# Kernel optimization log

Measured on AMD Instinct MI355X. Metric: run time of the kernel, lower is better.

Reference implementation:

```python
import jax, jax.numpy as jnp
import numpy as np

H, D = 12, 128          # heads, head_dim
DIM = 1536              # vid_dim == txt_dim == H*D
EPS = 1e-6


def _rmsnorm(x, w):
    # RMSNorm over last dim (head_dim) with learnable scale
    var = jnp.mean(jnp.square(x), axis=-1, keepdims=True)
    return x * jax.lax.rsqrt(var + EPS) * w


def setup_inputs() -> dict:
    key = jax.random.key(0)
    ks = jax.random.split(key, 16)
    B, Lv, Lt = 2, 2 * 24 * 40, 128
    inner = H * D
    s = 0.02
    inp = {
        "vid": jax.random.normal(ks[0], (B * Lv, DIM), jnp.float32),
        "txt": jax.random.normal(ks[1], (B * Lt, DIM), jnp.float32),
        "Wqkv_vid": jax.random.normal(ks[2], (DIM, 3 * inner), jnp.float32) * s,
        "bqkv_vid": jnp.zeros((3 * inner,), jnp.float32),
        "Wqkv_txt": jax.random.normal(ks[3], (DIM, 3 * inner), jnp.float32) * s,
        "bqkv_txt": jnp.zeros((3 * inner,), jnp.float32),
        "nq_vid": jnp.ones((D,), jnp.float32),
        "nk_vid": jnp.ones((D,), jnp.float32),
        "nq_txt": jnp.ones((D,), jnp.float32),
        "nk_txt": jnp.ones((D,), jnp.float32),
        "Wout_vid": jax.random.normal(ks[4], (inner, DIM), jnp.float32) * s,
        "bout_vid": jnp.zeros((DIM,), jnp.float32),
        "Wout_txt": jax.random.normal(ks[5], (inner, DIM), jnp.float32) * s,
        "bout_txt": jnp.zeros((DIM,), jnp.float32),
        # static per-sample shapes (numpy => usable as Python ints under jit)
        "vid_shape": np.array([[2, 24, 40], [2, 24, 40]], np.int64),
        "txt_shape": np.array([[128], [128]], np.int64),
    }
    return inp


def reference(vid, txt, Wqkv_vid, bqkv_vid, Wqkv_txt, bqkv_txt,
              nq_vid, nk_vid, nq_txt, nk_txt,
              Wout_vid, bout_vid, Wout_txt, bout_txt,
              vid_shape, txt_shape):
    B = vid_shape.shape[0]
    Lv = int(np.prod(vid_shape[0]))   # equal lengths across batch
    Lt = int(txt_shape[0, 0])

    # fused QKV projections (separate weights for vid/txt, shared_weights=False)
    vid_qkv = (vid @ Wqkv_vid + bqkv_vid).reshape(-1, 3, H, D)
    txt_qkv = (txt @ Wqkv_txt + bqkv_txt).reshape(-1, 3, H, D)
    vq, vk, vv = vid_qkv[:, 0], vid_qkv[:, 1], vid_qkv[:, 2]
    tq, tk, tv = txt_qkv[:, 0], txt_qkv[:, 1], txt_qkv[:, 2]

    # QK-norm (per-modality RMSNorm over head_dim)
    vq, tq = _rmsnorm(vq, nq_vid), _rmsnorm(tq, nq_txt)
    vk, tk = _rmsnorm(vk, nk_vid), _rmsnorm(tk, nk_txt)

    # multimodal packing: per sample, vid tokens then txt tokens (cu_seqlens over vid_len+txt_len)
    def pack(v, t):
        v = v.reshape(B, Lv, H, D)
        t = t.reshape(B, Lt, H, D)
        return jnp.concatenate([v, t], axis=1)  # [B, Lv+Lt, H, D]

    q = pack(vq, tq).astype(jnp.bfloat16)
    k = pack(vk, tk).astype(jnp.bfloat16)
    v = pack(vv, tv).astype(jnp.bfloat16)

    scale = 1.0 / np.sqrt(D)
    scores = jnp.einsum('blhd,bmhd->bhlm', q, k,
                        preferred_element_type=jnp.float32) * scale
    probs = jax.nn.softmax(scores, axis=-1)
    out = jnp.einsum('bhlm,bmhd->blhd', probs.astype(jnp.bfloat16), v,
                     preferred_element_type=jnp.float32).astype(vid.dtype)

    # unconcat + head merge
    out = out.reshape(B, Lv + Lt, H * D)
    vid_out = out[:, :Lv].reshape(B * Lv, H * D)
    txt_out = out[:, Lv:].reshape(B * Lt, H * D)

    vid_out = vid_out @ Wout_vid + bout_vid
    txt_out = txt_out @ Wout_txt + bout_txt
    return (vid_out, txt_out)
```

## Files before the change

### kernel.cpp

```cpp
#include <hip/hip_runtime.h>
#include <hip/hip_bf16.h>
#include <stdint.h>

typedef __attribute__((ext_vector_type(8))) short  short8;
typedef __attribute__((ext_vector_type(4))) float  f32x4;
typedef __attribute__((ext_vector_type(4))) unsigned int uint4v;
typedef __attribute__((ext_vector_type(4))) unsigned short ushort4v;

#define MFMA16(a,b,c) __builtin_amdgcn_mfma_f32_16x16x32_bf16((a),(b),(c),0,0,0)

#define AS1 __attribute__((address_space(1)))
#define AS3 __attribute__((address_space(3)))
static __device__ __forceinline__ void gload16(void* lds, const void* g) {
  __builtin_amdgcn_global_load_lds((AS1 const void*)g, (AS3 void*)lds, 16, 0, 0);
}

static __device__ __forceinline__ unsigned short f2bf(float x) {
  unsigned int u = __float_as_uint(x);
  u += 0x7fffu + ((u >> 16) & 1u);
  return (unsigned short)(u >> 16);
}
static __device__ __forceinline__ float bf2f(unsigned short h) {
  return __uint_as_float(((unsigned int)h) << 16);
}

#define HDS   12
#define DD    128
#define DIMK  1536
#define NIN   4608
#define LV    1920
#define LT    128
#define LL    2048
#define BB    2
#define MV    3840
#define MT    256
#define MTOT  4096

__global__ __launch_bounds__(256) void split_x(const float* __restrict__ vid,
                                               const float* __restrict__ txt,
                                               unsigned short* __restrict__ xhi) {
  size_t i = ((size_t)blockIdx.x * 256 + threadIdx.x) * 4;
  const size_t NV = (size_t)MV * DIMK;
  const float* src = (i < NV) ? (vid + i) : (txt + (i - NV));
  f32x4 v = *(const f32x4*)src;
  ushort4v hv;
#pragma unroll
  for (int j = 0; j < 4; ++j) hv[j] = f2bf(v[j]);
  *(ushort4v*)(xhi + i) = hv;
}

__global__ __launch_bounds__(256) void transpose_cast(const float* __restrict__ W,
                                                      unsigned short* __restrict__ Thi,
                                                      int K, int N) {
  __shared__ float tile[32][33];
  const int tx = threadIdx.x & 31, ty = threadIdx.x >> 5;
  const int k0 = blockIdx.y * 32, n0 = blockIdx.x * 32;
#pragma unroll
  for (int i = 0; i < 32; i += 8)
    tile[ty + i][tx] = W[(size_t)(k0 + ty + i) * N + n0 + tx];
  __syncthreads();
#pragma unroll
  for (int i = 0; i < 32; i += 8)
    Thi[(size_t)(n0 + ty + i) * K + k0 + tx] = f2bf(tile[tx][ty + i]);
}

__global__ __launch_bounds__(256) void vt_transpose(const unsigned short* __restrict__ v,
                                                    unsigned short* __restrict__ vtb) {
  __shared__ unsigned short tile[32][33];
  const int tx = threadIdx.x & 31, ty = threadIdx.x >> 5;
  const int bh = blockIdx.z;
  const int l0 = blockIdx.x * 32, d0 = blockIdx.y * 32;
  const size_t base = (size_t)bh * LL * DD;
#pragma unroll
  for (int i = 0; i < 32; i += 8)
    tile[ty + i][tx] = v[base + (size_t)(l0 + ty + i) * DD + d0 + tx];
  __syncthreads();
#pragma unroll
  for (int i = 0; i < 32; i += 8)
    vtb[base + (size_t)(d0 + ty + i) * LL + l0 + tx] = tile[tx][ty + i];
}

__device__ __forceinline__ void bf16_mainloop128(
    const unsigned short* __restrict__ Ahi, const unsigned short* __restrict__ Bhi,
    int m0, int n0,
    uint4v* __restrict__ sA, uint4v* __restrict__ sB,
    f32x4 (&acc)[4][4]) {
  const int t = threadIdx.x;
  const int lane = t & 63;
  const int w = t >> 6;
  const int wm = w >> 1, wn = w & 1;
  const int lr = lane & 15, lg = lane >> 4;
  const int sr = t >> 1;
  const int sc = (t & 1) * 2;
  const size_t arow = (size_t)(m0 + sr) * DIMK + sc * 8;
  const size_t brow = (size_t)(n0 + sr) * DIMK + sc * 8;
  const int slot0 = sc * 128 + sr, slot1 = (sc + 1) * 128 + sr;
  const int fA = lg * 128 + wm * 64 + lr;
  const int fB = lg * 128 + wn * 64 + lr;

  uint4v va0 = *(const uint4v*)(Ahi + arow);
  uint4v va1 = *(const uint4v*)(Ahi + arow + 8);
  uint4v vb0 = *(const uint4v*)(Bhi + brow);
  uint4v vb1 = *(const uint4v*)(Bhi + brow + 8);

  int cur = 0;
  for (int k0 = 0; k0 < DIMK; k0 += 32) {
    const int hs = cur * 512;
    sA[hs + slot0] = va0; sA[hs + slot1] = va1;
    sB[hs + slot0] = vb0; sB[hs + slot1] = vb1;
    if (k0 + 32 < DIMK) {
      va0 = *(const uint4v*)(Ahi + arow + k0 + 32);
      va1 = *(const uint4v*)(Ahi + arow + k0 + 40);
      vb0 = *(const uint4v*)(Bhi + brow + k0 + 32);
      vb1 = *(const uint4v*)(Bhi + brow + k0 + 40);
    }
    __syncthreads();
    short8 ah[4], bh[4];
#pragma unroll
    for (int i = 0; i < 4; ++i) {
      ah[i] = *(const short8*)&sA[hs + fA + i * 16];
      bh[i] = *(const short8*)&sB[hs + fB + i * 16];
    }
#pragma unroll
    for (int mi = 0; mi < 4; ++mi)
#pragma unroll
      for (int ni = 0; ni < 4; ++ni)
        acc[mi][ni] = MFMA16(ah[mi], bh[ni], acc[mi][ni]);
    cur ^= 1;
  }
}

__global__ __launch_bounds__(256) void gemm_qkv(
    const unsigned short* __restrict__ Xhi,
    const unsigned short* __restrict__ WvH, const unsigned short* __restrict__ WtH,
    const float* __restrict__ bias_v, const float* __restrict__ bias_t,
    const float* __restrict__ nq_v, const float* __restrict__ nk_v,
    const float* __restrict__ nq_t, const float* __restrict__ nk_t,
    unsigned short* __restrict__ qb, unsigned short* __restrict__ kb,
    unsigned short* __restrict__ vb) {
  __shared__ uint4v sA[1024], sB[1024];
  __shared__ float rowsq[2][128];
  const int t = threadIdx.x;
  const int lane = t & 63;
  const int w = t >> 6;
  const int wm = w >> 1, wn = w & 1;
  const int lr = lane & 15, lg = lane >> 4;
  const int bid = blockIdx.x;
  const int xcd = bid & 7, ii = bid >> 3;
  const int mt = xcd * 4 + (ii & 3), nt = ii >> 2;
  const int m0 = mt * 128, n0 = nt * 128;
  const bool istxt = (m0 >= MV);
  const unsigned short* WThi = istxt ? WtH : WvH;
  const float* bias = istxt ? bias_t : bias_v;
  const int Lmod = istxt ? LT : LV;
  const int loff = istxt ? LV : 0;
  const int mbase = istxt ? MV : 0;

  f32x4 acc[4][4];
#pragma unroll
  for (int mi = 0; mi < 4; ++mi)
#pragma unroll
    for (int ni = 0; ni < 4; ++ni) acc[mi][ni] = (f32x4){0.f, 0.f, 0.f, 0.f};

  bf16_mainloop128(Xhi, WThi, m0, n0, sA, sB, acc);

  const int s  = n0 / DIMK;
  const int hh = (n0 % DIMK) / DD;
#pragma unroll
  for (int ni = 0; ni < 4; ++ni) {
    float bv = bias[n0 + wn * 64 + ni * 16 + lr];
#pragma unroll
    for (int mi = 0; mi < 4; ++mi)
#pragma unroll
      for (int r = 0; r < 4; ++r) acc[mi][ni][r] += bv;
  }
  if (s < 2) {
    __syncthreads();
#pragma unroll
    for (int mi = 0; mi < 4; ++mi)
#pragma unroll
      for (int r = 0; r < 4; ++r) {
        float p = 0.f;
#pragma unroll
        for (int ni = 0; ni < 4; ++ni) p += acc[mi][ni][r] * acc[mi][ni][r];
        p += __shfl_xor(p, 1); p += __shfl_xor(p, 2);
        p += __shfl_xor(p, 4); p += __shfl_xor(p, 8);
        if (lr == 0) rowsq[wn][wm * 64 + mi * 16 + lg * 4 + r] = p;
      }
    __syncthreads();
    const float* nw = (s == 0) ? (istxt ? nq_t : nq_v) : (istxt ? nk_t : nk_v);
    float nwv[4];
#pragma unroll
    for (int ni = 0; ni < 4; ++ni) nwv[ni] = nw[wn * 64 + ni * 16 + lr];
#pragma unroll
    for (int mi = 0; mi < 4; ++mi)
#pragma unroll
      for (int r = 0; r < 4; ++r) {
        int row = wm * 64 + mi * 16 + lg * 4 + r;
        float a = (rowsq[0][row] + rowsq[1][row]) * (1.f / 128.f) + 1e-6f;
        float x = rsqrtf(a);
        x = x * (1.5f - 0.5f * a * x * x);
#pragma unroll
        for (int ni = 0; ni < 4; ++ni) acc[mi][ni][r] *= x * nwv[ni];
      }
  }
  unsigned short* dst = (s == 0) ? qb : ((s == 1) ? kb : vb);
#pragma unroll
  for (int mi = 0; mi < 4; ++mi)
#pragma unroll
    for (int r = 0; r < 4; ++r) {
      int mrow = m0 + wm * 64 + mi * 16 + lg * 4 + r - mbase;
      int bidx = (mrow >= Lmod) ? 1 : 0;
      int l = loff + mrow - bidx * Lmod;
      size_t rb2 = ((size_t)(bidx * HDS + hh) * LL + l) * DD;
#pragma unroll
      for (int ni = 0; ni < 4; ++ni) {
        int d = wn * 64 + ni * 16 + lr;
        dst[rb2 + d] = f2bf(acc[mi][ni][r]);
      }
    }
}

__global__ __launch_bounds__(256) void attn_kernel(
    const unsigned short* __restrict__ qb, const unsigned short* __restrict__ kb,
    const unsigned short* __restrict__ vt,
    unsigned short* __restrict__ aohi) {
  const int t = threadIdx.x;
  const int lane = t & 63, w = t >> 6;
  const int lr = lane & 15, lg = lane >> 4;
  const int bid = blockIdx.x;
  const int xcd = bid & 7, ii = bid >> 3;
  const int bh = xcd * 3 + (ii >> 5);
  const int qt = ii & 31;
  const int q0 = (qt * 4 + w) * 16;
  const size_t base = (size_t)bh * LL * DD;
  const float scale = 0.08838834764831845f;

  __shared__ __align__(16) unsigned short Kbuf[2][32 * 128];
  __shared__ __align__(16) unsigned short Vbuf[2][128 * 32];
  __shared__ __align__(16) unsigned short P[4][16 * 40];

  const char* kglob = (const char*)(kb + base);
  const char* vglob = (const char*)(vt + base);
  auto stageK = [&](int kt, int buf) {
    const char* gk = kglob + (size_t)kt * 32 * DD * 2;
#pragma unroll
    for (int is = 0; is < 2; ++is) {
      int Bl = is * 4096 + t * 16;
      int Bu = is * 4096 + w * 1024;
      int src = Bl ^ (((Bl >> 8) & 7) << 4);
      gload16((char*)Kbuf[buf] + Bu, gk + src);
    }
  };
  auto stageV = [&](int kt, int buf) {
    const char* gv = vglob + kt * 64;
#pragma unroll
    for (int is = 0; is < 2; ++is) {
      int Bl = is * 4096 + t * 16;
      int Bu = is * 4096 + w * 1024;
      int row = Bl >> 6;
      int ch  = ((Bl >> 4) & 3) ^ (row & 3);
      gload16((char*)Vbuf[buf] + Bu, gv + (size_t)row * (LL * 2) + ch * 16);
    }
  };
  auto readK = [&](int buf, int rr, int ks) -> short8 {
    int byte = rr * 256 + ((ks * 64 + lg * 16) ^ ((rr & 7) << 4));
    return *(const short8*)((const char*)Kbuf[buf] + byte);
  };
  auto readV = [&](int buf, int df) -> short8 {
    int row = df * 16 + lr;
    int byte = row * 64 + ((lg ^ (row & 3)) << 4);
    return *(const short8*)((const char*)Vbuf[buf] + byte);
  };

  short8 qf[4];
#pragma unroll
  for (int ks = 0; ks < 4; ++ks)
    qf[ks] = *(const short8*)(qb + base + (size_t)(q0 + lr) * DD + ks * 32 + lg * 8);

  f32x4 o[8];
#pragma unroll
  for (int i = 0; i < 8; ++i) o[i] = (f32x4){0.f, 0.f, 0.f, 0.f};
  float Z[4] = {0.f, 0.f, 0.f, 0.f};

  stageK(0, 0); stageV(0, 0);
  __syncthreads();
  for (int kt = 0; kt < LL / 32; ++kt) {
    const int cur = kt & 1;
    if (kt + 1 < LL / 32) { stageK(kt + 1, cur ^ 1); stageV(kt + 1, cur ^ 1); }
    f32x4 s0a = (f32x4){0.f, 0.f, 0.f, 0.f}, s0b = (f32x4){0.f, 0.f, 0.f, 0.f};
    f32x4 s1a = (f32x4){0.f, 0.f, 0.f, 0.f}, s1b = (f32x4){0.f, 0.f, 0.f, 0.f};
#pragma unroll
    for (int ks = 0; ks < 4; ++ks) {
      short8 k0f = readK(cur, lr, ks);
      short8 k1f = readK(cur, 16 + lr, ks);
      if (ks < 2) { s0a = MFMA16(qf[ks], k0f, s0a); s1a = MFMA16(qf[ks], k1f, s1a); }
      else        { s0b = MFMA16(qf[ks], k0f, s0b); s1b = MFMA16(qf[ks], k1f, s1b); }
    }
#pragma unroll
    for (int r = 0; r < 4; ++r) {
      float p0 = __expf((s0a[r] + s0b[r]) * scale);
      float p1 = __expf((s1a[r] + s1b[r]) * scale);
      Z[r] += p0 + p1;
      P[w][(lg * 4 + r) * 40 + lr]      = f2bf(p0);
      P[w][(lg * 4 + r) * 40 + 16 + lr] = f2bf(p1);
    }
    short8 pa = *(const short8*)&P[w][lr * 40 + lg * 8];
#pragma unroll
    for (int df = 0; df < 8; ++df) {
      short8 vf = readV(cur, df);
      o[df] = MFMA16(pa, vf, o[df]);
    }
    __syncthreads();
  }

  float invZ[4];
#pragma unroll
  for (int r = 0; r < 4; ++r) {
    Z[r] += __shfl_xor(Z[r], 1); Z[r] += __shfl_xor(Z[r], 2);
    Z[r] += __shfl_xor(Z[r], 4); Z[r] += __shfl_xor(Z[r], 8);
    invZ[r] = 1.0f / Z[r];
  }

  const int b = bh / HDS, h = bh % HDS;
#pragma unroll
  for (int df = 0; df < 8; ++df)
#pragma unroll
    for (int r = 0; r < 4; ++r) {
      int l = q0 + lg * 4 + r;
      size_t row = (l < LV) ? ((size_t)b * LV + l) : ((size_t)MV + b * LT + (l - LV));
      int col = h * DD + df * 16 + lr;
      aohi[row * DIMK + col] = f2bf(o[df][r] * invZ[r]);
    }
}

__global__ __launch_bounds__(256) void gemm_out(
    const unsigned short* __restrict__ Ahi,
    const unsigned short* __restrict__ WvH, const unsigned short* __restrict__ WtH,
    const float* __restrict__ bias_v, const float* __restrict__ bias_t,
    float* __restrict__ out) {
  __shared__ uint4v sA[1024], sB[1024];
  const int t = threadIdx.x;
  const int lane = t & 63;
  const int w = t >> 6;
  const int wm = w >> 1, wn = w & 1;
  const int lr = lane & 15, lg = lane >> 4;
  const int bid = blockIdx.x;
  const int xcd = bid & 7, ii = bid >> 3;
  const int mt = xcd * 4 + (ii & 3), nt = ii >> 2;
  const int m0 = mt * 128, n0 = nt * 128;
  const bool istxt = (m0 >= MV);
  const unsigned short* WThi = istxt ? WtH : WvH;
  const float* bias = istxt ? bias_t : bias_v;

  f32x4 acc[4][4];
#pragma unroll
  for (int mi = 0; mi < 4; ++mi)
#pragma unroll
    for (int ni = 0; ni < 4; ++ni) acc[mi][ni] = (f32x4){0.f, 0.f, 0.f, 0.f};

  bf16_mainloop128(Ahi, WThi, m0, n0, sA, sB, acc);

#pragma unroll
  for (int ni = 0; ni < 4; ++ni) {
    float bv = bias[n0 + wn * 64 + ni * 16 + lr];
#pragma unroll
    for (int mi = 0; mi < 4; ++mi)
#pragma unroll
      for (int r = 0; r < 4; ++r) {
        size_t row = (size_t)(m0 + wm * 64 + mi * 16 + lg * 4 + r);
        out[row * DIMK + n0 + wn * 64 + ni * 16 + lr] = acc[mi][ni][r] + bv;
      }
  }
}

extern "C" void kernel_launch(void* const* d_in, const int* in_sizes, int n_in,
                              void* d_out, int out_size, void* d_ws, size_t ws_size,
                              hipStream_t stream) {
  (void)in_sizes; (void)n_in; (void)out_size; (void)ws_size;
  const float* vid      = (const float*)d_in[0];
  const float* txt      = (const float*)d_in[1];
  const float* Wqkv_vid = (const float*)d_in[2];
  const float* bqkv_vid = (const float*)d_in[3];
  const float* Wqkv_txt = (const float*)d_in[4];
  const float* bqkv_txt = (const float*)d_in[5];
  const float* nq_vid   = (const float*)d_in[6];
  const float* nk_vid   = (const float*)d_in[7];
  const float* nq_txt   = (const float*)d_in[8];
  const float* nk_txt   = (const float*)d_in[9];
  const float* Wout_vid = (const float*)d_in[10];
  const float* bout_vid = (const float*)d_in[11];
  const float* Wout_txt = (const float*)d_in[12];
  const float* bout_txt = (const float*)d_in[13];
  float* out = (float*)d_out;

  char* ws = (char*)d_ws;
  size_t off = 0;
  auto alloc = [&](size_t bytes) { char* p = ws + off; off += (bytes + 255) & ~(size_t)255; return p; };

  const size_t SZ_X    = (size_t)MTOT * DIMK * 2;
  const size_t SZ_WQKV = (size_t)NIN * DIMK * 2;
  const size_t SZ_WOUT = (size_t)DIMK * DIMK * 2;
  const size_t SZ_QKVB = (size_t)BB * HDS * LL * DD * 2;

  unsigned short* Xhi   = (unsigned short*)alloc(SZ_X);
  unsigned short* WTqvH = (unsigned short*)alloc(SZ_WQKV);
  unsigned short* WTqtH = (unsigned short*)alloc(SZ_WQKV);
  unsigned short* WTovH = (unsigned short*)alloc(SZ_WOUT);
  unsigned short* WTotH = (unsigned short*)alloc(SZ_WOUT);
  unsigned short* QB    = (unsigned short*)alloc(SZ_QKVB);
  unsigned short* KB    = (unsigned short*)alloc(SZ_QKVB);
  unsigned short* VB    = (unsigned short*)alloc(SZ_QKVB);
  unsigned short* VT    = WTqvH;
  unsigned short* AOhi  = Xhi;

  split_x<<<dim3((MTOT * DIMK) / (256 * 4)), dim3(256), 0, stream>>>(vid, txt, Xhi);
  transpose_cast<<<dim3(NIN / 32, DIMK / 32), dim3(256), 0, stream>>>(Wqkv_vid, WTqvH, DIMK, NIN);
  transpose_cast<<<dim3(NIN / 32, DIMK / 32), dim3(256), 0, stream>>>(Wqkv_txt, WTqtH, DIMK, NIN);
  transpose_cast<<<dim3(DIMK / 32, DIMK / 32), dim3(256), 0, stream>>>(Wout_vid, WTovH, DIMK, DIMK);
  transpose_cast<<<dim3(DIMK / 32, DIMK / 32), dim3(256), 0, stream>>>(Wout_txt, WTotH, DIMK, DIMK);
  gemm_qkv<<<dim3(1152), dim3(256), 0, stream>>>(
      Xhi, WTqvH, WTqtH, bqkv_vid, bqkv_txt,
      nq_vid, nk_vid, nq_txt, nk_txt, QB, KB, VB);
  vt_transpose<<<dim3(LL / 32, DD / 32, BB * HDS), dim3(256), 0, stream>>>(VB, VT);
  attn_kernel<<<dim3(768), dim3(256), 0, stream>>>(QB, KB, VT, AOhi);
  gemm_out<<<dim3(384), dim3(256), 0, stream>>>(
      AOhi, WTovH, WTotH, bout_vid, bout_txt, out);
}
```

Baseline: 262.5 us.

## Use 256x128 tiles with 512 threads for QKV GEMM

Replaces the 128x128 QKV GEMM tile with a 256-row by 128-column tile computed by 8 waves in a 512-thread block, halving the grid to 576 blocks. Each loaded weight tile now serves twice as many rows, which cuts B-operand traffic and the number of weight reloads. The attention kernel is only moved in the file. The cost is larger LDS per block and fewer blocks, which lowers occupancy and leaves fewer blocks for load balancing across CUs.

Measured after the change: 243.6 us. 1.08x faster.

```diff
diff --git a/kernel.cpp b/kernel.cpp
--- a/kernel.cpp
+++ b/kernel.cpp
@@ -78,6 +78,259 @@
 #pragma unroll
   for (int i = 0; i < 32; i += 8)
     vtb[base + (size_t)(d0 + ty + i) * LL + l0 + tx] = tile[tx][ty + i];
+}
+
+__device__ __forceinline__ void bf16_mainloop256(
+    const unsigned short* __restrict__ Ahi, const unsigned short* __restrict__ Bhi,
+    int m0, int n0,
+    uint4v* __restrict__ sA, uint4v* __restrict__ sB,
+    f32x4 (&acc)[4][4]) {
+  const int t = threadIdx.x;
+  const int lane = t & 63;
+  const int w = t >> 6;
+  const int wm = w >> 1, wn = w & 1;
+  const int lr = lane & 15, lg = lane >> 4;
+  const int ra = t >> 1, ca = (t & 1) * 2;
+  const int rb = t >> 2, cb = t & 3;
+  const size_t arow = (size_t)(m0 + ra) * DIMK + ca * 8;
+  const size_t brow = (size_t)(n0 + rb) * DIMK + cb * 8;
+  const int sa0 = ca * 256 + ra, sa1 = (ca + 1) * 256 + ra;
+  const int sb0 = cb * 128 + rb;
+  const int fA = lg * 256 + wm * 64 + lr;
+  const int fB = lg * 128 + wn * 64 + lr;
+
+  uint4v va0 = *(const uint4v*)(Ahi + arow);
+  uint4v va1 = *(const uint4v*)(Ahi + arow + 8);
+  uint4v vb0 = *(const uint4v*)(Bhi + brow);
+
+  int cur = 0;
+  for (int k0 = 0; k0 < DIMK; k0 += 32) {
+    const int ha = cur * 1024, hb = cur * 512;
+    sA[ha + sa0] = va0; sA[ha + sa1] = va1;
+    sB[hb + sb0] = vb0;
+    if (k0 + 32 < DIMK) {
+      va0 = *(const uint4v*)(Ahi + arow + k0 + 32);
+      va1 = *(const uint4v*)(Ahi + arow + k0 + 40);
+      vb0 = *(const uint4v*)(Bhi + brow + k0 + 32);
+    }
+    __syncthreads();
+    short8 ah[4], bh[4];
+#pragma unroll
+    for (int i = 0; i < 4; ++i) {
+      ah[i] = *(const short8*)&sA[ha + fA + i * 16];
+      bh[i] = *(const short8*)&sB[hb + fB + i * 16];
+    }
+#pragma unroll
+    for (int mi = 0; mi < 4; ++mi)
+#pragma unroll
+      for (int ni = 0; ni < 4; ++ni)
+        acc[mi][ni] = MFMA16(ah[mi], bh[ni], acc[mi][ni]);
+    cur ^= 1;
+  }
+}
+
+__global__ __launch_bounds__(512) void gemm_qkv(
+    const unsigned short* __restrict__ Xhi,
+    const unsigned short* __restrict__ WvH, const unsigned short* __restrict__ WtH,
+    const float* __restrict__ bias_v, const float* __restrict__ bias_t,
+    const float* __restrict__ nq_v, const float* __restrict__ nk_v,
+    const float* __restrict__ nq_t, const float* __restrict__ nk_t,
+    unsigned short* __restrict__ qb, unsigned short* __restrict__ kb,
+    unsigned short* __restrict__ vb) {
+  __shared__ uint4v sA[2048], sB[1024];
+  __shared__ float rowsq[2][256];
+  const int t = threadIdx.x;
+  const int lane = t & 63;
+  const int w = t >> 6;
+  const int wm = w >> 1, wn = w & 1;
+  const int lr = lane & 15, lg = lane >> 4;
+  const int bid = blockIdx.x;
+  const int xcd = bid & 7, ii = bid >> 3;
+  const int mt = xcd * 2 + (ii & 1), nt = ii >> 1;
+  const int m0 = mt * 256, n0 = nt * 128;
+  const bool istxt = (m0 >= MV);
+  const unsigned short* WThi = istxt ? WtH : WvH;
+  const float* bias = istxt ? bias_t : bias_v;
+  const int Lmod = istxt ? LT : LV;
+  const int loff = istxt ? LV : 0;
+  const int mbase = istxt ? MV : 0;
+
+  f32x4 acc[4][4];
+#pragma unroll
+  for (int mi = 0; mi < 4; ++mi)
+#pragma unroll
+    for (int ni = 0; ni < 4; ++ni) acc[mi][ni] = (f32x4){0.f, 0.f, 0.f, 0.f};
+
+  bf16_mainloop256(Xhi, WThi, m0, n0, sA, sB, acc);
+
+  const int s  = n0 / DIMK;
+  const int hh = (n0 % DIMK) / DD;
+#pragma unroll
+  for (int ni = 0; ni < 4; ++ni) {
+    float bv = bias[n0 + wn * 64 + ni * 16 + lr];
+#pragma unroll
+    for (int mi = 0; mi < 4; ++mi)
+#pragma unroll
+      for (int r = 0; r < 4; ++r) acc[mi][ni][r] += bv;
+  }
+  if (s < 2) {
+    __syncthreads();
+#pragma unroll
+    for (int mi = 0; mi < 4; ++mi)
+#pragma unroll
+      for (int r = 0; r < 4; ++r) {
+        float p = 0.f;
+#pragma unroll
+        for (int ni = 0; ni < 4; ++ni) p += acc[mi][ni][r] * acc[mi][ni][r];
+        p += __shfl_xor(p, 1); p += __shfl_xor(p, 2);
+        p += __shfl_xor(p, 4); p += __shfl_xor(p, 8);
+        if (lr == 0) rowsq[wn][wm * 64 + mi * 16 + lg * 4 + r] = p;
+      }
+    __syncthreads();
+    const float* nw = (s == 0) ? (istxt ? nq_t : nq_v) : (istxt ? nk_t : nk_v);
+    float nwv[4];
+#pragma unroll
+    for (int ni = 0; ni < 4; ++ni) nwv[ni] = nw[wn * 64 + ni * 16 + lr];
+#pragma unroll
+    for (int mi = 0; mi < 4; ++mi)
+#pragma unroll
+      for (int r = 0; r < 4; ++r) {
+        int row = wm * 64 + mi * 16 + lg * 4 + r;
+        float a = (rowsq[0][row] + rowsq[1][row]) * (1.f / 128.f) + 1e-6f;
+        float x = rsqrtf(a);
+        x = x * (1.5f - 0.5f * a * x * x);
+#pragma unroll
+        for (int ni = 0; ni < 4; ++ni) acc[mi][ni][r] *= x * nwv[ni];
+      }
+  }
+  unsigned short* dst = (s == 0) ? qb : ((s == 1) ? kb : vb);
+#pragma unroll
+  for (int mi = 0; mi < 4; ++mi)
+#pragma unroll
+    for (int r = 0; r < 4; ++r) {
+      int mrow = m0 + wm * 64 + mi * 16 + lg * 4 + r - mbase;
+      int bidx = (mrow >= Lmod) ? 1 : 0;
+      int l = loff + mrow - bidx * Lmod;
+      size_t rb2 = ((size_t)(bidx * HDS + hh) * LL + l) * DD;
+#pragma unroll
+      for (int ni = 0; ni < 4; ++ni) {
+        int d = wn * 64 + ni * 16 + lr;
+        dst[rb2 + d] = f2bf(acc[mi][ni][r]);
+      }
+    }
+}
+
+__global__ __launch_bounds__(256) void attn_kernel(
+    const unsigned short* __restrict__ qb, const unsigned short* __restrict__ kb,
+    const unsigned short* __restrict__ vt,
+    unsigned short* __restrict__ aohi) {
+  const int t = threadIdx.x;
+  const int lane = t & 63, w = t >> 6;
+  const int lr = lane & 15, lg = lane >> 4;
+  const int bid = blockIdx.x;
+  const int xcd = bid & 7, ii = bid >> 3;
+  const int bh = xcd * 3 + (ii >> 5);
+  const int qt = ii & 31;
+  const int q0 = (qt * 4 + w) * 16;
+  const size_t base = (size_t)bh * LL * DD;
+  const float scale = 0.08838834764831845f;
+
+  __shared__ __align__(16) unsigned short Kbuf[2][32 * 128];
+  __shared__ __align__(16) unsigned short Vbuf[2][128 * 32];
+  __shared__ __align__(16) unsigned short P[4][16 * 40];
+
+  const char* kglob = (const char*)(kb + base);
+  const char* vglob = (const char*)(vt + base);
+  auto stageK = [&](int kt, int buf) {
+    const char* gk = kglob + (size_t)kt * 32 * DD * 2;
+#pragma unroll
+    for (int is = 0; is < 2; ++is) {
+      int Bl = is * 4096 + t * 16;
+      int Bu = is * 4096 + w * 1024;
+      int src = Bl ^ (((Bl >> 8) & 7) << 4);
+      gload16((char*)Kbuf[buf] + Bu, gk + src);
+    }
+  };
+  auto stageV = [&](int kt, int buf) {
+    const char* gv = vglob + kt * 64;
+#pragma unroll
+    for (int is = 0; is < 2; ++is) {
+      int Bl = is * 4096 + t * 16;
+      int Bu = is * 4096 + w * 1024;
+      int row = Bl >> 6;
+      int ch  = ((Bl >> 4) & 3) ^ (row & 3);
+      gload16((char*)Vbuf[buf] + Bu, gv + (size_t)row * (LL * 2) + ch * 16);
+    }
+  };
+  auto readK = [&](int buf, int rr, int ks) -> short8 {
+    int byte = rr * 256 + ((ks * 64 + lg * 16) ^ ((rr & 7) << 4));
+    return *(const short8*)((const char*)Kbuf[buf] + byte);
+  };
+  auto readV = [&](int buf, int df) -> short8 {
+    int row = df * 16 + lr;
+    int byte = row * 64 + ((lg ^ (row & 3)) << 4);
+    return *(const short8*)((const char*)Vbuf[buf] + byte);
+  };
+
+  short8 qf[4];
+#pragma unroll
+  for (int ks = 0; ks < 4; ++ks)
+    qf[ks] = *(const short8*)(qb + base + (size_t)(q0 + lr) * DD + ks * 32 + lg * 8);
+
+  f32x4 o[8];
+#pragma unroll
+  for (int i = 0; i < 8; ++i) o[i] = (f32x4){0.f, 0.f, 0.f, 0.f};
+  float Z[4] = {0.f, 0.f, 0.f, 0.f};
+
+  stageK(0, 0); stageV(0, 0);
+  __syncthreads();
+  for (int kt = 0; kt < LL / 32; ++kt) {
+    const int cur = kt & 1;
+    if (kt + 1 < LL / 32) { stageK(kt + 1, cur ^ 1); stageV(kt + 1, cur ^ 1); }
+    f32x4 s0a = (f32x4){0.f, 0.f, 0.f, 0.f}, s0b = (f32x4){0.f, 0.f, 0.f, 0.f};
+    f32x4 s1a = (f32x4){0.f, 0.f, 0.f, 0.f}, s1b = (f32x4){0.f, 0.f, 0.f, 0.f};
+#pragma unroll
+    for (int ks = 0; ks < 4; ++ks) {
+      short8 k0f = readK(cur, lr, ks);
+      short8 k1f = readK(cur, 16 + lr, ks);
+      if (ks < 2) { s0a = MFMA16(qf[ks], k0f, s0a); s1a = MFMA16(qf[ks], k1f, s1a); }
+      else        { s0b = MFMA16(qf[ks], k0f, s0b); s1b = MFMA16(qf[ks], k1f, s1b); }
+    }
+#pragma unroll
+    for (int r = 0; r < 4; ++r) {
+      float p0 = __expf((s0a[r] + s0b[r]) * scale);
+      float p1 = __expf((s1a[r] + s1b[r]) * scale);
+      Z[r] += p0 + p1;
+      P[w][(lg * 4 + r) * 40 + lr]      = f2bf(p0);
+      P[w][(lg * 4 + r) * 40 + 16 + lr] = f2bf(p1);
+    }
+    short8 pa = *(const short8*)&P[w][lr * 40 + lg * 8];
+#pragma unroll
+    for (int df = 0; df < 8; ++df) {
+      short8 vf = readV(cur, df);
+      o[df] = MFMA16(pa, vf, o[df]);
+    }
+    __syncthreads();
+  }
+
+  float invZ[4];
+#pragma unroll
+  for (int r = 0; r < 4; ++r) {
+    Z[r] += __shfl_xor(Z[r], 1); Z[r] += __shfl_xor(Z[r], 2);
+    Z[r] += __shfl_xor(Z[r], 4); Z[r] += __shfl_xor(Z[r], 8);
+    invZ[r] = 1.0f / Z[r];
+  }
+
+  const int b = bh / HDS, h = bh % HDS;
+#pragma unroll
+  for (int df = 0; df < 8; ++df)
+#pragma unroll
+    for (int r = 0; r < 4; ++r) {
+      int l = q0 + lg * 4 + r;
+      size_t row = (l < LV) ? ((size_t)b * LV + l) : ((size_t)MV + b * LT + (l - LV));
+      int col = h * DD + df * 16 + lr;
+      aohi[row * DIMK + col] = f2bf(o[df][r] * invZ[r]);
+    }
 }
 
 __device__ __forceinline__ void bf16_mainloop128(
@@ -128,210 +381,6 @@
         acc[mi][ni] = MFMA16(ah[mi], bh[ni], acc[mi][ni]);
     cur ^= 1;
   }
-}
-
-__global__ __launch_bounds__(256) void gemm_qkv(
-    const unsigned short* __restrict__ Xhi,
-    const unsigned short* __restrict__ WvH, const unsigned short* __restrict__ WtH,
-    const float* __restrict__ bias_v, const float* __restrict__ bias_t,
-    const float* __restrict__ nq_v, const float* __restrict__ nk_v,
-    const float* __restrict__ nq_t, const float* __restrict__ nk_t,
-    unsigned short* __restrict__ qb, unsigned short* __restrict__ kb,
-    unsigned short* __restrict__ vb) {
-  __shared__ uint4v sA[1024], sB[1024];
-  __shared__ float rowsq[2][128];
-  const int t = threadIdx.x;
-  const int lane = t & 63;
-  const int w = t >> 6;
-  const int wm = w >> 1, wn = w & 1;
-  const int lr = lane & 15, lg = lane >> 4;
-  const int bid = blockIdx.x;
-  const int xcd = bid & 7, ii = bid >> 3;
-  const int mt = xcd * 4 + (ii & 3), nt = ii >> 2;
-  const int m0 = mt * 128, n0 = nt * 128;
-  const bool istxt = (m0 >= MV);
-  const unsigned short* WThi = istxt ? WtH : WvH;
-  const float* bias = istxt ? bias_t : bias_v;
-  const int Lmod = istxt ? LT : LV;
-  const int loff = istxt ? LV : 0;
-  const int mbase = istxt ? MV : 0;
-
-  f32x4 acc[4][4];
-#pragma unroll
-  for (int mi = 0; mi < 4; ++mi)
-#pragma unroll
-    for (int ni = 0; ni < 4; ++ni) acc[mi][ni] = (f32x4){0.f, 0.f, 0.f, 0.f};
-
-  bf16_mainloop128(Xhi, WThi, m0, n0, sA, sB, acc);
-
-  const int s  = n0 / DIMK;
-  const int hh = (n0 % DIMK) / DD;
-#pragma unroll
-  for (int ni = 0; ni < 4; ++ni) {
-    float bv = bias[n0 + wn * 64 + ni * 16 + lr];
-#pragma unroll
-    for (int mi = 0; mi < 4; ++mi)
-#pragma unroll
-      for (int r = 0; r < 4; ++r) acc[mi][ni][r] += bv;
-  }
-  if (s < 2) {
-    __syncthreads();
-#pragma unroll
-    for (int mi = 0; mi < 4; ++mi)
-#pragma unroll
-      for (int r = 0; r < 4; ++r) {
-        float p = 0.f;
-#pragma unroll
-        for (int ni = 0; ni < 4; ++ni) p += acc[mi][ni][r] * acc[mi][ni][r];
-        p += __shfl_xor(p, 1); p += __shfl_xor(p, 2);
-        p += __shfl_xor(p, 4); p += __shfl_xor(p, 8);
-        if (lr == 0) rowsq[wn][wm * 64 + mi * 16 + lg * 4 + r] = p;
-      }
-    __syncthreads();
-    const float* nw = (s == 0) ? (istxt ? nq_t : nq_v) : (istxt ? nk_t : nk_v);
-    float nwv[4];
-#pragma unroll
-    for (int ni = 0; ni < 4; ++ni) nwv[ni] = nw[wn * 64 + ni * 16 + lr];
-#pragma unroll
-    for (int mi = 0; mi < 4; ++mi)
-#pragma unroll
-      for (int r = 0; r < 4; ++r) {
-        int row = wm * 64 + mi * 16 + lg * 4 + r;
-        float a = (rowsq[0][row] + rowsq[1][row]) * (1.f / 128.f) + 1e-6f;
-        float x = rsqrtf(a);
-        x = x * (1.5f - 0.5f * a * x * x);
-#pragma unroll
-        for (int ni = 0; ni < 4; ++ni) acc[mi][ni][r] *= x * nwv[ni];
-      }
-  }
-  unsigned short* dst = (s == 0) ? qb : ((s == 1) ? kb : vb);
-#pragma unroll
-  for (int mi = 0; mi < 4; ++mi)
-#pragma unroll
-    for (int r = 0; r < 4; ++r) {
-      int mrow = m0 + wm * 64 + mi * 16 + lg * 4 + r - mbase;
-      int bidx = (mrow >= Lmod) ? 1 : 0;
-      int l = loff + mrow - bidx * Lmod;
-      size_t rb2 = ((size_t)(bidx * HDS + hh) * LL + l) * DD;
-#pragma unroll
-      for (int ni = 0; ni < 4; ++ni) {
-        int d = wn * 64 + ni * 16 + lr;
-        dst[rb2 + d] = f2bf(acc[mi][ni][r]);
-      }
-    }
-}
-
-__global__ __launch_bounds__(256) void attn_kernel(
-    const unsigned short* __restrict__ qb, const unsigned short* __restrict__ kb,
-    const unsigned short* __restrict__ vt,
-    unsigned short* __restrict__ aohi) {
-  const int t = threadIdx.x;
-  const int lane = t & 63, w = t >> 6;
-  const int lr = lane & 15, lg = lane >> 4;
-  const int bid = blockIdx.x;
-  const int xcd = bid & 7, ii = bid >> 3;
-  const int bh = xcd * 3 + (ii >> 5);
-  const int qt = ii & 31;
-  const int q0 = (qt * 4 + w) * 16;
-  const size_t base = (size_t)bh * LL * DD;
-  const float scale = 0.08838834764831845f;
-
-  __shared__ __align__(16) unsigned short Kbuf[2][32 * 128];
-  __shared__ __align__(16) unsigned short Vbuf[2][128 * 32];
-  __shared__ __align__(16) unsigned short P[4][16 * 40];
-
-  const char* kglob = (const char*)(kb + base);
-  const char* vglob = (const char*)(vt + base);
-  auto stageK = [&](int kt, int buf) {
-    const char* gk = kglob + (size_t)kt * 32 * DD * 2;
-#pragma unroll
-    for (int is = 0; is < 2; ++is) {
-      int Bl = is * 4096 + t * 16;
-      int Bu = is * 4096 + w * 1024;
-      int src = Bl ^ (((Bl >> 8) & 7) << 4);
-      gload16((char*)Kbuf[buf] + Bu, gk + src);
-    }
-  };
-  auto stageV = [&](int kt, int buf) {
-    const char* gv = vglob + kt * 64;
-#pragma unroll
-    for (int is = 0; is < 2; ++is) {
-      int Bl = is * 4096 + t * 16;
-      int Bu = is * 4096 + w * 1024;
-      int row = Bl >> 6;
-      int ch  = ((Bl >> 4) & 3) ^ (row & 3);
-      gload16((char*)Vbuf[buf] + Bu, gv + (size_t)row * (LL * 2) + ch * 16);
-    }
-  };
-  auto readK = [&](int buf, int rr, int ks) -> short8 {
-    int byte = rr * 256 + ((ks * 64 + lg * 16) ^ ((rr & 7) << 4));
-    return *(const short8*)((const char*)Kbuf[buf] + byte);
-  };
-  auto readV = [&](int buf, int df) -> short8 {
-    int row = df * 16 + lr;
-    int byte = row * 64 + ((lg ^ (row & 3)) << 4);
-    return *(const short8*)((const char*)Vbuf[buf] + byte);
-  };
-
-  short8 qf[4];
-#pragma unroll
-  for (int ks = 0; ks < 4; ++ks)
-    qf[ks] = *(const short8*)(qb + base + (size_t)(q0 + lr) * DD + ks * 32 + lg * 8);
-
-  f32x4 o[8];
-#pragma unroll
-  for (int i = 0; i < 8; ++i) o[i] = (f32x4){0.f, 0.f, 0.f, 0.f};
-  float Z[4] = {0.f, 0.f, 0.f, 0.f};
-
-  stageK(0, 0); stageV(0, 0);
-  __syncthreads();
-  for (int kt = 0; kt < LL / 32; ++kt) {
-    const int cur = kt & 1;
-    if (kt + 1 < LL / 32) { stageK(kt + 1, cur ^ 1); stageV(kt + 1, cur ^ 1); }
-    f32x4 s0a = (f32x4){0.f, 0.f, 0.f, 0.f}, s0b = (f32x4){0.f, 0.f, 0.f, 0.f};
-    f32x4 s1a = (f32x4){0.f, 0.f, 0.f, 0.f}, s1b = (f32x4){0.f, 0.f, 0.f, 0.f};
-#pragma unroll
-    for (int ks = 0; ks < 4; ++ks) {
-      short8 k0f = readK(cur, lr, ks);
-      short8 k1f = readK(cur, 16 + lr, ks);
-      if (ks < 2) { s0a = MFMA16(qf[ks], k0f, s0a); s1a = MFMA16(qf[ks], k1f, s1a); }
-      else        { s0b = MFMA16(qf[ks], k0f, s0b); s1b = MFMA16(qf[ks], k1f, s1b); }
-    }
-#pragma unroll
-    for (int r = 0; r < 4; ++r) {
-      float p0 = __expf((s0a[r] + s0b[r]) * scale);
-      float p1 = __expf((s1a[r] + s1b[r]) * scale);
-      Z[r] += p0 + p1;
-      P[w][(lg * 4 + r) * 40 + lr]      = f2bf(p0);
-      P[w][(lg * 4 + r) * 40 + 16 + lr] = f2bf(p1);
-    }
-    short8 pa = *(const short8*)&P[w][lr * 40 + lg * 8];
-#pragma unroll
-    for (int df = 0; df < 8; ++df) {
-      short8 vf = readV(cur, df);
-      o[df] = MFMA16(pa, vf, o[df]);
-    }
-    __syncthreads();
-  }
-
-  float invZ[4];
-#pragma unroll
-  for (int r = 0; r < 4; ++r) {
-    Z[r] += __shfl_xor(Z[r], 1); Z[r] += __shfl_xor(Z[r], 2);
-    Z[r] += __shfl_xor(Z[r], 4); Z[r] += __shfl_xor(Z[r], 8);
-    invZ[r] = 1.0f / Z[r];
-  }
-
-  const int b = bh / HDS, h = bh % HDS;
-#pragma unroll
-  for (int df = 0; df < 8; ++df)
-#pragma unroll
-    for (int r = 0; r < 4; ++r) {
-      int l = q0 + lg * 4 + r;
-      size_t row = (l < LV) ? ((size_t)b * LV + l) : ((size_t)MV + b * LT + (l - LV));
-      int col = h * DD + df * 16 + lr;
-      aohi[row * DIMK + col] = f2bf(o[df][r] * invZ[r]);
-    }
 }
 
 __global__ __launch_bounds__(256) void gemm_out(
@@ -419,7 +468,7 @@
   transpose_cast<<<dim3(NIN / 32, DIMK / 32), dim3(256), 0, stream>>>(Wqkv_txt, WTqtH, DIMK, NIN);
   transpose_cast<<<dim3(DIMK / 32, DIMK / 32), dim3(256), 0, stream>>>(Wout_vid, WTovH, DIMK, DIMK);
   transpose_cast<<<dim3(DIMK / 32, DIMK / 32), dim3(256), 0, stream>>>(Wout_txt, WTotH, DIMK, DIMK);
-  gemm_qkv<<<dim3(1152), dim3(256), 0, stream>>>(
+  gemm_qkv<<<dim3(576), dim3(512), 0, stream>>>(
       Xhi, WTqvH, WTqtH, bqkv_vid, bqkv_txt,
       nq_vid, nk_vid, nq_txt, nk_txt, QB, KB, VB);
   vt_transpose<<<dim3(LL / 32, DD / 32, BB * HDS), dim3(256), 0, stream>>>(VB, VT);
```
